# Kernel optimization log

Hardware: AMD Instinct MI355X
Metric: run time of the kernel (lower is better)

## Reference

```python
import jax, jax.numpy as jnp
import numpy as np

B, NF, G, H, W = 4, 64, 8, 96, 96
K, KK = 3, 9
CG = NF // G  # channels per deformable group


def _conv3(x, w, b):
    # 3x3 conv, stride 1, pad 1, NCHW/OIHW
    y = jax.lax.conv_general_dilated(x, w, (1, 1), ((1, 1), (1, 1)),
                                     dimension_numbers=('NCHW', 'OIHW', 'NCHW'))
    return y + b[None, :, None, None]


def _lrelu(x):
    return jnp.where(x >= 0, x, 0.1 * x)


def _up2(x):
    # bilinear x2 upsample, align_corners=False (PyTorch semantics: src clamped at 0, indices clamped at n-1)
    def up_axis(x, axis):
        n = x.shape[axis]
        src = jnp.maximum((jnp.arange(2 * n, dtype=jnp.float32) + 0.5) / 2.0 - 0.5, 0.0)
        i0 = jnp.floor(src).astype(jnp.int32)
        i1 = jnp.minimum(i0 + 1, n - 1)
        t = (src - i0.astype(jnp.float32))
        x0 = jnp.take(x, i0, axis=axis)
        x1 = jnp.take(x, i1, axis=axis)
        shp = [1] * x.ndim
        shp[axis] = 2 * n
        t = t.reshape(shp)
        return x0 * (1.0 - t) + x1 * t
    return up_axis(up_axis(x, 2), 3)


def _dcn(x, off_feat, w_om, b_om, w_d, b_d):
    # Modulated deformable conv (DCNv2, separate offset input), 3x3, stride 1, pad 1, dil 1,
    # conv groups = 1, deformable groups = G.
    b, c, h, w = x.shape
    om = _conv3(off_feat, w_om, b_om)                     # [B, 3*G*KK, H, W]
    o_y, o_x, m = jnp.split(om, 3, axis=1)                # each [B, G*KK, H, W]
    off_y = o_y.reshape(b, G, KK, h, w)
    off_x = o_x.reshape(b, G, KK, h, w)
    mask = jax.nn.sigmoid(m).reshape(b, G, KK, h, w)

    dy = (jnp.arange(KK, dtype=jnp.float32) // K - 1.0)   # [-1,-1,-1,0,0,0,1,1,1]
    dx = (jnp.arange(KK, dtype=jnp.float32) % K - 1.0)
    ys = jnp.arange(h, dtype=jnp.float32)
    xs = jnp.arange(w, dtype=jnp.float32)
    # sampling positions: [B, G, KK, H, W]
    py = off_y + ys[None, None, None, :, None] + dy[None, None, :, None, None]
    px = off_x + xs[None, None, None, None, :] + dx[None, None, :, None, None]

    y0f = jnp.floor(py); x0f = jnp.floor(px)
    ty = py - y0f; tx = px - x0f
    y0 = y0f.astype(jnp.int32); x0 = x0f.astype(jnp.int32)
    y1 = y0 + 1; x1 = x0 + 1

    xg = x.reshape(b, G, CG, h * w)  # per-deformable-group channels

    def samp(iy, ix):
        valid = ((iy >= 0) & (iy < h) & (ix >= 0) & (ix < w)).astype(x.dtype)  # [B,G,KK,H,W]
        idx = jnp.clip(iy, 0, h - 1) * w + jnp.clip(ix, 0, w - 1)
        idxf = idx.reshape(b, G, 1, KK * h * w)
        v = jnp.take_along_axis(xg, jnp.broadcast_to(idxf, (b, G, CG, KK * h * w)), axis=3)
        return v.reshape(b, G, CG, KK, h, w) * valid[:, :, None]

    w00 = ((1 - ty) * (1 - tx))[:, :, None]
    w01 = ((1 - ty) * tx)[:, :, None]
    w10 = (ty * (1 - tx))[:, :, None]
    w11 = (ty * tx)[:, :, None]
    cols = (samp(y0, x0) * w00 + samp(y0, x1) * w01 +
            samp(y1, x0) * w10 + samp(y1, x1) * w11)
    cols = cols * mask[:, :, None]                        # modulation
    cols = cols.reshape(b, c, KK, h, w)
    out = jnp.einsum('bckhw,ock->bohw', cols, w_d.reshape(c, c, KK))
    return out + b_d[None, :, None, None]


def setup_inputs() -> dict:
    key = jax.random.key(0)
    ks = jax.random.split(key, 20)
    s = 0.05
    inp = {
        'src0': jax.random.normal(ks[0], (B, NF, H, W), jnp.float32),
        'src1': jax.random.normal(ks[1], (B, NF, H, W), jnp.float32),
        'last_offset': jax.random.normal(ks[2], (B, NF, H // 2, W // 2), jnp.float32),
        'last_feature': jax.random.normal(ks[3], (B, NF, H // 2, W // 2), jnp.float32),
        'w_off1': jax.random.normal(ks[4], (NF, 2 * NF, 3, 3), jnp.float32) * s,
        'b_off1': jax.random.normal(ks[5], (NF,), jnp.float32) * s,
        'w_off2': jax.random.normal(ks[6], (NF, 2 * NF, 3, 3), jnp.float32) * s,
        'b_off2': jax.random.normal(ks[7], (NF,), jnp.float32) * s,
        'w_off3': jax.random.normal(ks[8], (NF, NF, 3, 3), jnp.float32) * s,
        'b_off3': jax.random.normal(ks[9], (NF,), jnp.float32) * s,
        'w_om': jax.random.normal(ks[10], (3 * G * KK, NF, 3, 3), jnp.float32) * s,
        'b_om': jax.random.normal(ks[11], (3 * G * KK,), jnp.float32) * s,
        'w_dcn': jax.random.normal(ks[12], (NF, NF, 3, 3), jnp.float32) * s,
        'b_dcn': jax.random.normal(ks[13], (NF,), jnp.float32) * s,
        'w_fea': jax.random.normal(ks[14], (NF, 2 * NF, 3, 3), jnp.float32) * s,
        'b_fea': jax.random.normal(ks[15], (NF,), jnp.float32) * s,
    }
    return inp


def reference(src0, src1, last_offset, last_feature,
              w_off1, b_off1, w_off2, b_off2, w_off3, b_off3,
              w_om, b_om, w_dcn, b_dcn, w_fea, b_fea):
    offset = _lrelu(_conv3(jnp.concatenate([src0, src1], axis=1), w_off1, b_off1))
    lo = _up2(last_offset)
    offset = _lrelu(_conv3(jnp.concatenate([offset, lo * 2.0], axis=1), w_off2, b_off2))
    offset = _lrelu(_conv3(offset, w_off3, b_off3))
    feature = _dcn(src0, offset, w_om, b_om, w_dcn, b_dcn)
    lf = _up2(last_feature)
    feature = _conv3(jnp.concatenate([feature, lf], axis=1), w_fea, b_fea)
    feature = _lrelu(feature)
    return (offset, feature)
```

## Files before the change

kernel.cpp:

```cpp
#include <hip/hip_runtime.h>
#include <hip/hip_fp16.h>
#include <math.h>

typedef __attribute__((ext_vector_type(8))) short bf16x8;
typedef __attribute__((ext_vector_type(8))) _Float16 half8;
typedef __attribute__((ext_vector_type(4))) float f32x4;
typedef __attribute__((ext_vector_type(4))) int int4v;

#define GL_LDS16(g, l) __builtin_amdgcn_global_load_lds( \
    (const __attribute__((address_space(1))) void*)(g), \
    (__attribute__((address_space(3))) void*)(l), 16, 0, 0)

__device__ __forceinline__ ushort f2bf(float f) {
    union { float f; unsigned u; } v; v.f = f;
    unsigned r = (v.u + 0x7fffu + ((v.u >> 16) & 1u)) >> 16;
    return (ushort)r;
}
__device__ __forceinline__ float bf2f(ushort h) {
    union { unsigned u; float f; } v; v.u = ((unsigned)h) << 16;
    return v.f;
}

__device__ __forceinline__ void prep_one(const float* __restrict__ w,
        ushort* __restrict__ wp, int u, int Cin, int CoutR, int CoutP) {
    int oc = u % CoutP; int t = u / CoutP;
    int kg = t & 3; t >>= 2;
    int kk = t % 9; int cc = t / 9;
    alignas(16) ushort tmp[8];
    for (int j = 0; j < 8; ++j) {
        int c = cc * 32 + kg * 8 + j;
        float v = (oc < CoutR) ? w[((size_t)oc * Cin + c) * 9 + kk] : 0.f;
        tmp[j] = f2bf(v);
    }
    *(int4v*)(wp + (size_t)u * 8) = *(int4v*)tmp;
}

__global__ __launch_bounds__(256) void pack_combo_k(
        const float* __restrict__ s0, const float* __restrict__ s1,
        const float* __restrict__ lo, const float* __restrict__ lf,
        const float* __restrict__ w1, const float* __restrict__ w2,
        const float* __restrict__ w3, const float* __restrict__ wom,
        const float* __restrict__ wd, const float* __restrict__ wf,
        const float* __restrict__ bom,
        ushort* __restrict__ xin1, ushort* __restrict__ xin2,
        ushort* __restrict__ xin4, ushort* __restrict__ xg1,
        ushort* __restrict__ w1p, ushort* __restrict__ w2p,
        ushort* __restrict__ w3p, ushort* __restrict__ womp,
        ushort* __restrict__ wdp, ushort* __restrict__ wfp,
        float* __restrict__ bpp, float* __restrict__ zg) {
    int b = blockIdx.y;
    int z = blockIdx.z;
    int px = blockIdx.x * 64 + (threadIdx.x & 63);
    int u = threadIdx.x >> 6;
    if (z == 0) {
        for (int half = 0; half < 2; ++half) {
            int cg = u + half * 4;
            float vals[16];
            alignas(16) ushort tmp[16];
            for (int i = 0; i < 16; ++i) {
                int c = cg * 16 + i;
                float v = (c < 64) ? s0[((size_t)(b * 64 + c)) * 9216 + px]
                                   : s1[((size_t)(b * 64 + c - 64)) * 9216 + px];
                vals[i] = v;
                tmp[i] = f2bf(v);
            }
            ushort* dst = xin1 + ((size_t)(b * 9216) + px) * 128 + cg * 16;
            *(int4v*)dst = *(int4v*)&tmp[0];
            *(int4v*)(dst + 8) = *(int4v*)&tmp[8];
            if (half == 0) {
                alignas(16) __half th[16];
                for (int i = 0; i < 16; ++i) th[i] = __float2half(vals[i]);
                ushort* gdst = xg1 + (((size_t)(b * 8 + cg * 2) * 9216) + px) * 8;
                *(int4v*)gdst = *(int4v*)&th[0];
                *(int4v*)(gdst + 9216 * 8) = *(int4v*)&th[8];
            }
        }
    } else if (z < 3) {
        const float* in = (z == 1) ? lo : lf;
        float scale = (z == 1) ? 2.0f : 1.0f;
        ushort* xo = (z == 1) ? xin2 : xin4;
        int y = px / 96, x = px % 96;
        float sy = fmaxf(y * 0.5f - 0.25f, 0.f);
        float sx = fmaxf(x * 0.5f - 0.25f, 0.f);
        int y0 = (int)sy, x0 = (int)sx;
        float ty = sy - (float)y0, tx = sx - (float)x0;
        int y1 = min(y0 + 1, 47), x1 = min(x0 + 1, 47);
        alignas(16) ushort tmp[16];
        for (int i = 0; i < 16; ++i) {
            int c = u * 16 + i;
            const float* p = in + ((size_t)(b * 64 + c)) * 2304;
            float v00 = p[y0 * 48 + x0], v01 = p[y0 * 48 + x1];
            float v10 = p[y1 * 48 + x0], v11 = p[y1 * 48 + x1];
            float v = (v00 * (1.f - tx) + v01 * tx) * (1.f - ty)
                    + (v10 * (1.f - tx) + v11 * tx) * ty;
            tmp[i] = f2bf(v * scale);
        }
        ushort* dst = xo + ((size_t)(b * 9216) + px) * 128 + 64 + u * 16;
        *(int4v*)dst = *(int4v*)&tmp[0];
        *(int4v*)(dst + 8) = *(int4v*)&tmp[8];
    } else {
        int uu = (blockIdx.x + 144 * blockIdx.y) * 256 + threadIdx.x;
        if (uu < 9216) prep_one(w1, w1p, uu, 128, 64, 64);
        else if (uu < 18432) prep_one(w2, w2p, uu - 9216, 128, 64, 64);
        else if (uu < 23040) prep_one(w3, w3p, uu - 18432, 64, 64, 64);
        else if (uu < 43776) {
            int v = uu - 23040;
            int ocp = v % 288; int t = v / 288;
            int kg = t & 3; t >>= 2;
            int kk = t % 9; int cc = t / 9;
            int t3 = ocp & 3, gkkp = ocp >> 2;
            alignas(16) ushort tmp[8];
            for (int j = 0; j < 8; ++j) {
                int c = cc * 32 + kg * 8 + j;
                float vv = (t3 < 3)
                    ? wom[((size_t)(t3 * 72 + gkkp) * 64 + c) * 9 + kk] : 0.f;
                tmp[j] = f2bf(vv);
            }
            *(int4v*)(womp + (size_t)v * 8) = *(int4v*)tmp;
        } else if (uu < 48384) {
            int v = uu - 43776;
            int oc = v & 63; int gkk = v >> 6;
            int g = gkk / 9, kk = gkk % 9;
            alignas(16) __half tmp[8];
            for (int j = 0; j < 8; ++j)
                tmp[j] = __float2half(wd[((size_t)oc * 64 + g * 8 + j) * 9 + kk]);
            *(int4v*)(wdp + (size_t)v * 8) = *(int4v*)tmp;
        } else if (uu < 57600) prep_one(wf, wfp, uu - 48384, 128, 64, 64);
        else if (uu < 57888) {
            int ocp = uu - 57600; int t3 = ocp & 3, gkkp = ocp >> 2;
            bpp[ocp] = (t3 < 3) ? bom[t3 * 72 + gkkp] : 0.f;
        } else if (uu < 57904) zg[uu - 57888] = 0.f;
    }
}

template<int CIN, int MT, int NZ, bool LRELU, bool ST_F32, bool ST_CHL>
__global__ __launch_bounds__(256, 4) void conv_mfma_k(
        const ushort* __restrict__ xin,
        const ushort* __restrict__ wp,
        const float* __restrict__ bias,
        float* __restrict__ outf,
        ushort* __restrict__ chl,
        const ushort* __restrict__ zg,
        int CoutR, int CoutP, int ochs, int ocoff) {
    constexpr int SL = CIN / 64;
    constexpr int OCN = MT * 16;
    __shared__ ushort s_act[SL][7200];

    int tid = threadIdx.x;
    int wv = tid >> 6, ln = tid & 63;
    int l15 = ln & 15, l4 = ln >> 4;

    constexpr int TOTAL = 144 * 4 * NZ;
    constexpr int CHUNK = TOTAL / 8;
    int bid = blockIdx.x;
    int nid = (bid & 7) * CHUNK + (bid >> 3);
    int zc = nid % NZ; int r1 = nid / NZ;
    int tile = r1 % 144; int b = r1 / 144;
    int bx = (tile % 12) * 8, by = (tile / 12) * 8;
    int oc0 = zc * OCN;

    int px_l = wv * 16 + l15;
    int py = px_l >> 3, pxx = px_l & 7;
    int b_base = (py * 10 + pxx) * 72 + l4 * 8;

    const ushort* wlane = wp + ((size_t)l4 * CoutP + oc0 + l15) * 8;

    f32x4 acc[MT];
#pragma unroll
    for (int mt = 0; mt < MT; ++mt) acc[mt] = (f32x4){0.f, 0.f, 0.f, 0.f};

    auto STAGE = [&](int sl, int buf) {
        for (int i = tid; i < 900; i += 256) {
            int p = i / 9, q = i - p * 9;
            int gy = by + (p / 10) - 1, gx = bx + (p % 10) - 1;
            const ushort* src = zg;
            if (q < 8 && (unsigned)gy < 96u && (unsigned)gx < 96u)
                src = xin + ((size_t)(b * 9216 + gy * 96 + gx) * CIN
                             + sl * 64 + q * 8);
            GL_LDS16(src, s_act[buf] + (size_t)i * 8);
        }
    };

    STAGE(0, 0);
    __syncthreads();
#pragma unroll
    for (int sl = 0; sl < SL; ++sl) {
        if (sl + 1 < SL) STAGE(sl + 1, (sl + 1) & 1);
#pragma unroll
        for (int cc2 = 0; cc2 < 2; ++cc2) {
#pragma unroll
            for (int kk = 0; kk < 9; ++kk) {
                bf16x8 bfrag = *(const bf16x8*)(s_act[sl & (SL - 1)] + b_base +
                                   ((kk / 3) * 10 + (kk % 3)) * 72 + cc2 * 32);
#pragma unroll
                for (int mt = 0; mt < MT; ++mt) {
                    bf16x8 af = *(const bf16x8*)(wlane +
                        ((size_t)((sl * 2 + cc2) * 36 + kk * 4) * CoutP + mt * 16) * 8);
                    acc[mt] = __builtin_amdgcn_mfma_f32_16x16x32_bf16(
                        af, bfrag, acc[mt], 0, 0, 0);
                }
            }
        }
        if (sl + 1 < SL) __syncthreads();
    }

    int gy = by + py, gx = bx + pxx;
    size_t pxg = (size_t)b * 9216 + gy * 96 + gx;
#pragma unroll
    for (int mt = 0; mt < MT; ++mt) {
        int ocb = oc0 + mt * 16 + l4 * 4;
        ushort hb[4];
#pragma unroll
        for (int r = 0; r < 4; ++r) {
            int oc = ocb + r;
            float v = acc[mt][r] + ((oc < CoutR) ? bias[oc] : 0.f);
            if (LRELU) v = (v >= 0.f) ? v : 0.1f * v;
            hb[r] = f2bf(v);
            if (ST_F32 && oc < CoutR)
                outf[((size_t)b * CoutR + oc) * 9216 + gy * 96 + gx] = v;
        }
        if (ST_CHL && ocb < CoutR) {
            uint2 pk;
            pk.x = (uint)hb[0] | ((uint)hb[1] << 16);
            pk.y = (uint)hb[2] | ((uint)hb[3] << 16);
            *(uint2*)(chl + pxg * ochs + ocoff + ocb) = pk;
        }
    }
}

__global__ __launch_bounds__(192, 2) void dcn_fused_k(
        const ushort* __restrict__ xoff,
        const ushort* __restrict__ xg1,
        const ushort* __restrict__ womp,
        const float* __restrict__ bpp,
        const ushort* __restrict__ wdp,
        const float* __restrict__ bd, ushort* __restrict__ chl,
        const ushort* __restrict__ zg) {
    __shared__ ushort s_x[816 * 8];
    __shared__ ushort s_zone[3 * 2 * 4 * 64 * 8];
    __shared__ float s_red[2][2][64][17];
    int tid = threadIdx.x;
    int kq = tid >> 6, ln = tid & 63;
    int l15 = ln & 15, l4 = ln >> 4;
    int bid = blockIdx.x;
    int nid = (bid & 7) * 144 + (bid >> 3);
    int pxb = nid % 288; int b = nid / 288;
    int px0 = pxb * 32;
    int y = px0 / 96, x0 = px0 % 96;

    for (int i = tid; i < 816; i += 192) {
        int P = i >> 3, s8 = i & 7;
        int q = s8 ^ (P & 7);
        int ry = y - 1 + P / 34, rx = x0 - 1 + P % 34;
        const ushort* src = zg;
        if ((unsigned)ry < 96u && (unsigned)rx < 96u)
            src = xoff + (((size_t)b * 9216 + ry * 96 + rx) * 64 + q * 8);
        GL_LDS16(src, s_x + (size_t)i * 8);
    }
    __syncthreads();

    f32x4 acc0[4], acc1[4];
#pragma unroll
    for (int mt = 0; mt < 4; ++mt) {
        acc0[mt] = (f32x4){0.f, 0.f, 0.f, 0.f};
        acc1[mt] = (f32x4){0.f, 0.f, 0.f, 0.f};
    }

    float cwb[2][4];

    auto PREP = [&](int s, int gx, const f32x4& aom) {
        int st = kq * 6 + s;
        int gkk = st * 4 + l4;
        int g = gkk / 9, kk = gkk - g * 9;
        int bofs = st * 16 + l4 * 4;
        int xx = x0 + gx * 16 + l15;
        float oy = aom[0] + bpp[bofs];
        float ox = aom[1] + bpp[bofs + 1];
        float mm = 1.f / (1.f + __expf(-(aom[2] + bpp[bofs + 2])));
        float py = oy + (float)(y + kk / 3 - 1);
        float pxf = ox + (float)(xx + kk % 3 - 1);
        float yf = floorf(py), xf = floorf(pxf);
        float fy = py - yf, fx = pxf - xf;
        int iy0 = (int)yf, ix0 = (int)xf;
        int iy1 = iy0 + 1, ix1 = ix0 + 1;
        float vy0 = ((unsigned)iy0 < 96u) ? 1.f : 0.f;
        float vy1 = ((unsigned)iy1 < 96u) ? 1.f : 0.f;
        float vx0 = ((unsigned)ix0 < 96u) ? 1.f : 0.f;
        float vx1 = ((unsigned)ix1 < 96u) ? 1.f : 0.f;
        int r0 = min(max(iy0, 0), 95), r1 = min(max(iy1, 0), 95);
        int lb = min(max(ix0, 0), 94);
        float h0 = (float)min(max(ix0 - lb, 0), 1);
        float h1 = (float)min(max(ix1 - lb, 0), 1);
        float wx0 = (1.f - fx) * vx0, wx1 = fx * vx1;
        float xw0 = wx0 * (1.f - h0) + wx1 * (1.f - h1);
        float xw1 = wx0 * h0 + wx1 * h1;
        float rw0 = (1.f - fy) * vy0 * mm, rw1 = fy * vy1 * mm;
        cwb[gx][0] = rw0 * xw0; cwb[gx][1] = rw0 * xw1;
        cwb[gx][2] = rw1 * xw0; cwb[gx][3] = rw1 * xw1;
        const ushort* gp = xg1 + ((size_t)(b * 8 + g) * 9216) * 8;
        const ushort* p0 = gp + ((size_t)(r0 * 96 + lb)) * 8;
        const ushort* p1 = gp + ((size_t)(r1 * 96 + lb)) * 8;
        ushort* zb = s_zone + ((size_t)((kq * 2 + gx) * 4) * 64 + ln) * 8;
        GL_LDS16(p0,     zb);
        GL_LDS16(p0 + 8, zb + 64 * 8);
        GL_LDS16(p1,     zb + 128 * 8);
        GL_LDS16(p1 + 8, zb + 192 * 8);
    };

    auto CONSUME2 = [&](int s) {
        asm volatile("s_waitcnt vmcnt(0)" ::: "memory");
        __builtin_amdgcn_sched_barrier(0);
        half8 bu[2];
#pragma unroll
        for (int gx = 0; gx < 2; ++gx) {
            const ushort* zb = s_zone + ((size_t)((kq * 2 + gx) * 4) * 64 + ln) * 8;
            union { int4v v; __half2 h2[4]; } a0, a1, b0c, b1c;
            a0.v  = *(const int4v*)zb;
            a1.v  = *(const int4v*)(zb + 64 * 8);
            b0c.v = *(const int4v*)(zb + 128 * 8);
            b1c.v = *(const int4v*)(zb + 192 * 8);
            __half2 w0 = __float2half2_rn(cwb[gx][0]);
            __half2 w1 = __float2half2_rn(cwb[gx][1]);
            __half2 w2 = __float2half2_rn(cwb[gx][2]);
            __half2 w3 = __float2half2_rn(cwb[gx][3]);
            union { __half2 h2[4]; half8 v; } buv;
#pragma unroll
            for (int j = 0; j < 4; ++j) {
                __half2 t = __hmul2(a0.h2[j], w0);
                t = __hfma2(a1.h2[j], w1, t);
                t = __hfma2(b0c.h2[j], w2, t);
                t = __hfma2(b1c.h2[j], w3, t);
                buv.h2[j] = t;
            }
            bu[gx] = buv.v;
        }
        int gkk = (kq * 6 + s) * 4 + l4;
#pragma unroll
        for (int mt = 0; mt < 4; ++mt) {
            half8 af = *(const half8*)(wdp +
                ((size_t)gkk * 64 + mt * 16 + l15) * 8);
            acc0[mt] = __builtin_amdgcn_mfma_f32_16x16x32_f16(
                af, bu[0], acc0[mt], 0, 0, 0);
            acc1[mt] = __builtin_amdgcn_mfma_f32_16x16x32_f16(
                af, bu[1], acc1[mt], 0, 0, 0);
        }
    };

#pragma unroll
    for (int s = 0; s < 7; ++s) {
        f32x4 aom0 = (f32x4){0.f, 0.f, 0.f, 0.f};
        f32x4 aom1 = (f32x4){0.f, 0.f, 0.f, 0.f};
        if (s < 6) {
#pragma unroll
            for (int kk = 0; kk < 9; ++kk) {
                int ky = kk / 3, kx = kk % 3;
#pragma unroll
                for (int cc = 0; cc < 2; ++cc) {
                    int c8 = cc * 4 + l4;
                    int P0 = ky * 34 + l15 + kx;
                    int P1 = P0 + 16;
                    bf16x8 bf0 = *(const bf16x8*)(s_x +
                        ((size_t)(P0 * 8 + (c8 ^ (P0 & 7)))) * 8);
                    bf16x8 bf1 = *(const bf16x8*)(s_x +
                        ((size_t)(P1 * 8 + (c8 ^ (P1 & 7)))) * 8);
                    bf16x8 af = *(const bf16x8*)(womp +
                        ((size_t)(((cc * 9 + kk) * 4 + l4) * 288)
                         + (kq * 6 + s) * 16 + l15) * 8);
                    aom0 = __builtin_amdgcn_mfma_f32_16x16x32_bf16(
                        af, bf0, aom0, 0, 0, 0);
                    aom1 = __builtin_amdgcn_mfma_f32_16x16x32_bf16(
                        af, bf1, aom1, 0, 0, 0);
                }
            }
        }
        if (s >= 1) CONSUME2(s - 1);
        if (s < 6) {
            PREP(s, 0, aom0);
            PREP(s, 1, aom1);
        }
    }

    if (kq) {
#pragma unroll
        for (int mt = 0; mt < 4; ++mt)
#pragma unroll
            for (int r = 0; r < 4; ++r) {
                s_red[kq - 1][0][ln][mt * 4 + r] = acc0[mt][r];
                s_red[kq - 1][1][ln][mt * 4 + r] = acc1[mt][r];
            }
    }
    __syncthreads();
    if (!kq) {
#pragma unroll
        for (int gx = 0; gx < 2; ++gx) {
            size_t pb = (size_t)b * 9216 + px0 + gx * 16 + l15;
#pragma unroll
            for (int mt = 0; mt < 4; ++mt) {
                ushort hb[4];
#pragma unroll
                for (int r = 0; r < 4; ++r) {
                    int oc = mt * 16 + l4 * 4 + r;
                    float a = gx ? acc1[mt][r] : acc0[mt][r];
                    float v = a + s_red[0][gx][ln][mt * 4 + r]
                            + s_red[1][gx][ln][mt * 4 + r] + bd[oc];
                    hb[r] = f2bf(v);
                }
                uint2 pk;
                pk.x = (uint)hb[0] | ((uint)hb[1] << 16);
                pk.y = (uint)hb[2] | ((uint)hb[3] << 16);
                *(uint2*)(chl + pb * 128 + mt * 16 + l4 * 4) = pk;
            }
        }
    }
}

extern "C" void kernel_launch(void* const* d_in, const int* in_sizes, int n_in,
                              void* d_out, int out_size, void* d_ws, size_t ws_size,
                              hipStream_t stream) {
    const float* src0  = (const float*)d_in[0];
    const float* src1  = (const float*)d_in[1];
    const float* l_off = (const float*)d_in[2];
    const float* l_fea = (const float*)d_in[3];
    const float* w1 = (const float*)d_in[4];   const float* b1 = (const float*)d_in[5];
    const float* w2 = (const float*)d_in[6];   const float* b2 = (const float*)d_in[7];
    const float* w3 = (const float*)d_in[8];   const float* b3 = (const float*)d_in[9];
    const float* wom = (const float*)d_in[10]; const float* bom = (const float*)d_in[11];
    const float* wd = (const float*)d_in[12];  const float* bd = (const float*)d_in[13];
    const float* wf = (const float*)d_in[14];  const float* bf = (const float*)d_in[15];

    char* W = (char*)d_ws;
    ushort* xin1 = (ushort*)(W + 0);
    ushort* xin2 = (ushort*)(W + 9437184);
    ushort* xoff = (ushort*)(W + 9437184);
    ushort* xin3 = (ushort*)(W + 18874368);
    ushort* xin4 = (ushort*)(W + 44826624);
    ushort* xg1  = (ushort*)(W + 54263808);
    ushort* w1p  = (ushort*)(W + 58982400);
    ushort* w2p  = (ushort*)(W + 59129856);
    ushort* w3p  = (ushort*)(W + 59277312);
    ushort* womp = (ushort*)(W + 59351040);
    ushort* wdp  = (ushort*)(W + 59682816);
    ushort* wfp  = (ushort*)(W + 59756544);
    float*  bpp  = (float*)(W + 59904000);
    float*  zgrd = (float*)(W + 59905152);

    float* out_off = (float*)d_out;
    float* out_fea = out_off + (size_t)4 * 64 * 9216;

    pack_combo_k<<<dim3(144, 4, 4), 256, 0, stream>>>(
        src0, src1, l_off, l_fea, w1, w2, w3, wom, wd, wf, bom,
        xin1, xin2, xin4, xg1, w1p, w2p, w3p, womp, wdp, wfp, bpp, zgrd);

    const ushort* zg = (const ushort*)zgrd;
    conv_mfma_k<128, 2, 2, true, false, true><<<1152, 256, 0, stream>>>(
        xin1, w1p, b1, nullptr, xin2, zg, 64, 64, 128, 0);
    conv_mfma_k<128, 2, 2, true, false, true><<<1152, 256, 0, stream>>>(
        xin2, w2p, b2, nullptr, xin3, zg, 64, 64, 64, 0);
    conv_mfma_k<64, 2, 2, true, true, true><<<1152, 256, 0, stream>>>(
        xin3, w3p, b3, out_off, xoff, zg, 64, 64, 64, 0);
    dcn_fused_k<<<1152, 192, 0, stream>>>(xoff, xg1, womp, bpp, wdp, bd,
                                          xin4, zg);
    conv_mfma_k<128, 2, 2, true, true, false><<<1152, 256, 0, stream>>>(
        xin4, wfp, bf, out_fea, nullptr, zg, 64, 64, 0, 0);
}
```

Before: 125.8 us.

## Enlarge conv tiles to 16x8 pixels and swizzle LDS activation layout

New measurement: 123.7 us, median of 2. Within noise of the previous version (-1.7%).

```diff
diff --git a/kernel.cpp b/kernel.cpp
--- a/kernel.cpp
+++ b/kernel.cpp
@@ -133,8 +133,8 @@
     }
 }
 
-template<int CIN, int MT, int NZ, bool LRELU, bool ST_F32, bool ST_CHL>
-__global__ __launch_bounds__(256, 4) void conv_mfma_k(
+template<int CIN, int NZ, bool LRELU, bool ST_F32, bool ST_CHL>
+__global__ __launch_bounds__(256, 3) void conv_mfma_k(
         const ushort* __restrict__ xin,
         const ushort* __restrict__ wp,
         const float* __restrict__ bias,
@@ -143,39 +143,38 @@
         const ushort* __restrict__ zg,
         int CoutR, int CoutP, int ochs, int ocoff) {
     constexpr int SL = CIN / 64;
-    constexpr int OCN = MT * 16;
-    __shared__ ushort s_act[SL][7200];
+    __shared__ ushort s_act[SL][11520];
 
     int tid = threadIdx.x;
     int wv = tid >> 6, ln = tid & 63;
     int l15 = ln & 15, l4 = ln >> 4;
 
-    constexpr int TOTAL = 144 * 4 * NZ;
+    constexpr int TOTAL = 72 * 4 * NZ;
     constexpr int CHUNK = TOTAL / 8;
     int bid = blockIdx.x;
     int nid = (bid & 7) * CHUNK + (bid >> 3);
     int zc = nid % NZ; int r1 = nid / NZ;
-    int tile = r1 % 144; int b = r1 / 144;
-    int bx = (tile % 12) * 8, by = (tile / 12) * 8;
-    int oc0 = zc * OCN;
-
-    int px_l = wv * 16 + l15;
-    int py = px_l >> 3, pxx = px_l & 7;
-    int b_base = (py * 10 + pxx) * 72 + l4 * 8;
+    int tile = r1 % 72; int b = r1 / 72;
+    int bx = (tile % 6) * 16, by = (tile / 6) * 8;
+    int oc0 = zc * 32;
 
     const ushort* wlane = wp + ((size_t)l4 * CoutP + oc0 + l15) * 8;
 
-    f32x4 acc[MT];
-#pragma unroll
-    for (int mt = 0; mt < MT; ++mt) acc[mt] = (f32x4){0.f, 0.f, 0.f, 0.f};
+    f32x4 acc[2][2];
+#pragma unroll
+    for (int g = 0; g < 2; ++g)
+#pragma unroll
+        for (int mt = 0; mt < 2; ++mt)
+            acc[g][mt] = (f32x4){0.f, 0.f, 0.f, 0.f};
 
     auto STAGE = [&](int sl, int buf) {
-        for (int i = tid; i < 900; i += 256) {
-            int p = i / 9, q = i - p * 9;
-            int gy = by + (p / 10) - 1, gx = bx + (p % 10) - 1;
+        for (int i = tid; i < 1440; i += 256) {
+            int P = i >> 3, s8 = i & 7;
+            int q = s8 ^ (P & 7);
+            int ry = by - 1 + P / 18, rx = bx - 1 + P % 18;
             const ushort* src = zg;
-            if (q < 8 && (unsigned)gy < 96u && (unsigned)gx < 96u)
-                src = xin + ((size_t)(b * 9216 + gy * 96 + gx) * CIN
+            if ((unsigned)ry < 96u && (unsigned)rx < 96u)
+                src = xin + ((size_t)(b * 9216 + ry * 96 + rx) * CIN
                              + sl * 64 + q * 8);
             GL_LDS16(src, s_act[buf] + (size_t)i * 8);
         }
@@ -188,42 +187,53 @@
         if (sl + 1 < SL) STAGE(sl + 1, (sl + 1) & 1);
 #pragma unroll
         for (int cc2 = 0; cc2 < 2; ++cc2) {
+            int c8 = cc2 * 4 + l4;
 #pragma unroll
             for (int kk = 0; kk < 9; ++kk) {
-                bf16x8 bfrag = *(const bf16x8*)(s_act[sl & (SL - 1)] + b_base +
-                                   ((kk / 3) * 10 + (kk % 3)) * 72 + cc2 * 32);
-#pragma unroll
-                for (int mt = 0; mt < MT; ++mt) {
+                int ky = kk / 3, kx = kk % 3;
+                int P0 = (wv * 2 + ky) * 18 + l15 + kx;
+                int P1 = P0 + 18;
+                bf16x8 bf0 = *(const bf16x8*)(s_act[sl & (SL - 1)] +
+                    ((size_t)(P0 * 8 + (c8 ^ (P0 & 7)))) * 8);
+                bf16x8 bf1 = *(const bf16x8*)(s_act[sl & (SL - 1)] +
+                    ((size_t)(P1 * 8 + (c8 ^ (P1 & 7)))) * 8);
+#pragma unroll
+                for (int mt = 0; mt < 2; ++mt) {
                     bf16x8 af = *(const bf16x8*)(wlane +
                         ((size_t)((sl * 2 + cc2) * 36 + kk * 4) * CoutP + mt * 16) * 8);
-                    acc[mt] = __builtin_amdgcn_mfma_f32_16x16x32_bf16(
-                        af, bfrag, acc[mt], 0, 0, 0);
+                    acc[0][mt] = __builtin_amdgcn_mfma_f32_16x16x32_bf16(
+                        af, bf0, acc[0][mt], 0, 0, 0);
+                    acc[1][mt] = __builtin_amdgcn_mfma_f32_16x16x32_bf16(
+                        af, bf1, acc[1][mt], 0, 0, 0);
                 }
             }
         }
         if (sl + 1 < SL) __syncthreads();
     }
 
-    int gy = by + py, gx = bx + pxx;
-    size_t pxg = (size_t)b * 9216 + gy * 96 + gx;
-#pragma unroll
-    for (int mt = 0; mt < MT; ++mt) {
-        int ocb = oc0 + mt * 16 + l4 * 4;
-        ushort hb[4];
-#pragma unroll
-        for (int r = 0; r < 4; ++r) {
-            int oc = ocb + r;
-            float v = acc[mt][r] + ((oc < CoutR) ? bias[oc] : 0.f);
-            if (LRELU) v = (v >= 0.f) ? v : 0.1f * v;
-            hb[r] = f2bf(v);
-            if (ST_F32 && oc < CoutR)
-                outf[((size_t)b * CoutR + oc) * 9216 + gy * 96 + gx] = v;
-        }
-        if (ST_CHL && ocb < CoutR) {
-            uint2 pk;
-            pk.x = (uint)hb[0] | ((uint)hb[1] << 16);
-            pk.y = (uint)hb[2] | ((uint)hb[3] << 16);
-            *(uint2*)(chl + pxg * ochs + ocoff + ocb) = pk;
+#pragma unroll
+    for (int g = 0; g < 2; ++g) {
+        int gy = by + wv * 2 + g, gxp = bx + l15;
+        size_t pxg = (size_t)b * 9216 + gy * 96 + gxp;
+#pragma unroll
+        for (int mt = 0; mt < 2; ++mt) {
+            int ocb = oc0 + mt * 16 + l4 * 4;
+            ushort hb[4];
+#pragma unroll
+            for (int r = 0; r < 4; ++r) {
+                int oc = ocb + r;
+                float v = acc[g][mt][r] + ((oc < CoutR) ? bias[oc] : 0.f);
+                if (LRELU) v = (v >= 0.f) ? v : 0.1f * v;
+                hb[r] = f2bf(v);
+                if (ST_F32 && oc < CoutR)
+                    outf[((size_t)b * CoutR + oc) * 9216 + gy * 96 + gxp] = v;
+            }
+            if (ST_CHL && ocb < CoutR) {
+                uint2 pk;
+                pk.x = (uint)hb[0] | ((uint)hb[1] << 16);
+                pk.y = (uint)hb[2] | ((uint)hb[3] << 16);
+                *(uint2*)(chl + pxg * ochs + ocoff + ocb) = pk;
+            }
         }
     }
 }
@@ -452,14 +462,14 @@
         xin1, xin2, xin4, xg1, w1p, w2p, w3p, womp, wdp, wfp, bpp, zgrd);
 
     const ushort* zg = (const ushort*)zgrd;
-    conv_mfma_k<128, 2, 2, true, false, true><<<1152, 256, 0, stream>>>(
+    conv_mfma_k<128, 2, true, false, true><<<576, 256, 0, stream>>>(
         xin1, w1p, b1, nullptr, xin2, zg, 64, 64, 128, 0);
-    conv_mfma_k<128, 2, 2, true, false, true><<<1152, 256, 0, stream>>>(
+    conv_mfma_k<128, 2, true, false, true><<<576, 256, 0, stream>>>(
         xin2, w2p, b2, nullptr, xin3, zg, 64, 64, 64, 0);
-    conv_mfma_k<64, 2, 2, true, true, true><<<1152, 256, 0, stream>>>(
+    conv_mfma_k<64, 2, true, true, true><<<576, 256, 0, stream>>>(
         xin3, w3p, b3, out_off, xoff, zg, 64, 64, 64, 0);
     dcn_fused_k<<<1152, 192, 0, stream>>>(xoff, xg1, womp, bpp, wdp, bd,
                                           xin4, zg);
-    conv_mfma_k<128, 2, 2, true, true, false><<<1152, 256, 0, stream>>>(
+    conv_mfma_k<128, 2, true, true, false><<<576, 256, 0, stream>>>(
         xin4, wfp, bf, out_fea, nullptr, zg, 64, 64, 0, 0);
 }
```
